# Kernel tuning notes

Measured on AMD Instinct MI355X. Metric: run time of the kernel, lower is better.

The kernel has to match this reference:

```python
import jax, jax.numpy as jnp
import numpy as np

N_NODES = 100000
N_EDGES = 200000
N_GRAPHS = 4096
NODE_DIM = 256
OUT_DIM = 768
LAYERS = 4
NODE_FEATS = 9
EDGE_FEATS = 3
NODE_VOCAB = 119  # max categorical size across node features (padded)
EDGE_VOCAB = 22   # max categorical size across edge features (padded)


def setup_inputs() -> dict:
    key = jax.random.key(0)
    ks = jax.random.split(key, 16)
    x_cat = jax.random.randint(ks[0], (N_NODES, NODE_FEATS), 0, 2)
    edge_attr = jax.random.randint(ks[1], (N_EDGES, EDGE_FEATS), 0, 2)
    edge_index = jax.random.randint(ks[2], (2, N_EDGES), 0, N_NODES)
    batch = jnp.sort(jax.random.randint(ks[3], (N_NODES,), 0, N_GRAPHS))
    s = 0.02
    node_emb = jax.random.normal(ks[4], (NODE_FEATS, NODE_VOCAB, NODE_DIM), jnp.float32) * s
    edge_emb = jax.random.normal(ks[5], (EDGE_FEATS, EDGE_VOCAB, NODE_DIM), jnp.float32) * s
    W1 = jax.random.normal(ks[6], (LAYERS, NODE_DIM, 2 * NODE_DIM), jnp.float32) * s
    b1 = jnp.zeros((LAYERS, 2 * NODE_DIM), jnp.float32)
    W2 = jax.random.normal(ks[7], (LAYERS, 2 * NODE_DIM, NODE_DIM), jnp.float32) * s
    b2 = jnp.zeros((LAYERS, NODE_DIM), jnp.float32)
    pW1 = jax.random.normal(ks[8], (NODE_DIM, NODE_DIM), jnp.float32) * s
    pb1 = jnp.zeros((NODE_DIM,), jnp.float32)
    pW2 = jax.random.normal(ks[9], (NODE_DIM, OUT_DIM), jnp.float32) * s
    pb2 = jnp.zeros((OUT_DIM,), jnp.float32)
    return {
        "x_cat": x_cat, "edge_attr": edge_attr, "edge_index": edge_index, "batch": batch,
        "node_emb": node_emb, "edge_emb": edge_emb,
        "W1": W1, "b1": b1, "W2": W2, "b2": b2,
        "pW1": pW1, "pb1": pb1, "pW2": pW2, "pb2": pb2,
    }


def _encode(tables, idx):
    # tables: [F, V, D], idx: [N, F] -> sum over features of embedding lookups -> [N, D]
    return jnp.sum(jax.vmap(lambda tbl, i: tbl[i], in_axes=(0, 1))(tables, idx), axis=0)


def reference(x_cat, edge_attr, edge_index, batch, node_emb, edge_emb,
              W1, b1, W2, b2, pW1, pb1, pW2, pb2):
    x = _encode(node_emb, x_cat)          # [N, D]
    e = _encode(edge_emb, edge_attr)      # [E, D]
    src, dst = edge_index[0], edge_index[1]
    for l in range(LAYERS):
        # GINEConv: aggr = sum_{j in N(i)} relu(x_j + e_ij); out = mlp((1+eps)*x_i + aggr), eps=0
        msg = jax.nn.relu(x[src] + e)                                  # [E, D]
        agg = jax.ops.segment_sum(msg, dst, num_segments=N_NODES)     # [N, D]
        h = x + agg
        h = jax.nn.relu(h @ W1[l] + b1[l]) @ W2[l] + b2[l]
        x = jax.nn.relu(h)
    g = jax.ops.segment_sum(x, batch, num_segments=N_GRAPHS)          # [G, D]
    g = jax.nn.relu(g @ pW1 + pb1) @ pW2 + pb2                         # [G, OUT]
    norm = jnp.maximum(jnp.linalg.norm(g, axis=-1, keepdims=True), 1e-12)
    return g / norm
```

## Files before the change

kernel.cpp:

```cpp
#include <hip/hip_runtime.h>

#define N_NODES 100000
#define N_NODES_PAD 100032
#define N_EDGES 200000
#define N_GRAPHS 4096
#define D 256
#define D2 512
#define OUTD 768
#define LAYERS 4
#define NODE_FEATS 9
#define EDGE_FEATS 3
#define NODE_VOCAB 119
#define EDGE_VOCAB 22
#define BM 64
#define GB 8

typedef __attribute__((ext_vector_type(8))) short bf16x8;
typedef __attribute__((ext_vector_type(4))) float f32x4;
typedef unsigned short ushort_t;
typedef unsigned int uint_t;

__device__ __forceinline__ ushort_t f2b(float f) {
    union { float f; uint_t u; } x; x.f = f;
    uint_t r = (x.u + 0x7FFFu + ((x.u >> 16) & 1u)) >> 16;
    return (ushort_t)r;
}
__device__ __forceinline__ float b2f(ushort_t u) {
    union { uint_t u; float f; } x; x.u = ((uint_t)u) << 16;
    return x.f;
}

__device__ __forceinline__ int lower_bound_i(const int* a, int n, int v) {
    int lo = 0, hi = n;
    while (lo < hi) { int mid = (lo + hi) >> 1; if (a[mid] < v) lo = mid + 1; else hi = mid; }
    return lo;
}

__global__ __launch_bounds__(256) void encode_nodes_k(const int* __restrict__ xcat,
                                                      const float* __restrict__ tab,
                                                      ushort_t* __restrict__ X) {
    int n = blockIdx.x, d = threadIdx.x;
    float acc = 0.f;
#pragma unroll
    for (int f = 0; f < NODE_FEATS; ++f) {
        int idx = xcat[n * NODE_FEATS + f];
        acc += tab[((size_t)f * NODE_VOCAB + idx) * D + d];
    }
    X[(size_t)n * D + d] = f2b(acc);
}

__global__ __launch_bounds__(256) void count_k(const int* __restrict__ eidx, int* deg) {
    int e = blockIdx.x * 256 + threadIdx.x;
    if (e < N_EDGES) atomicAdd(&deg[eidx[N_EDGES + e]], 1);
}

#define SCAN_B 1024
__global__ __launch_bounds__(256) void scan1_k(const int* __restrict__ deg,
                                               int* __restrict__ excl, int* __restrict__ bsum) {
    __shared__ int sh[256];
    int b = blockIdx.x, t = threadIdx.x;
    int base = b * SCAN_B + t * 4;
    int d0 = (base + 0) < N_NODES ? deg[base + 0] : 0;
    int d1 = (base + 1) < N_NODES ? deg[base + 1] : 0;
    int d2 = (base + 2) < N_NODES ? deg[base + 2] : 0;
    int d3 = (base + 3) < N_NODES ? deg[base + 3] : 0;
    int s = d0 + d1 + d2 + d3;
    sh[t] = s; __syncthreads();
    for (int off = 1; off < 256; off <<= 1) {
        int x = (t >= off) ? sh[t - off] : 0;
        __syncthreads();
        sh[t] += x;
        __syncthreads();
    }
    int incl = sh[t];
    int ex = incl - s;
    if (base + 0 < N_NODES) excl[base + 0] = ex;
    if (base + 1 < N_NODES) excl[base + 1] = ex + d0;
    if (base + 2 < N_NODES) excl[base + 2] = ex + d0 + d1;
    if (base + 3 < N_NODES) excl[base + 3] = ex + d0 + d1 + d2;
    if (t == 255) bsum[b] = incl;
}

__global__ void scan2_k(int* bsum, int nb) {
    __shared__ int sh[128];
    int t = threadIdx.x;
    int v = (t < nb) ? bsum[t] : 0;
    sh[t] = v; __syncthreads();
    for (int off = 1; off < 128; off <<= 1) {
        int x = (t >= off) ? sh[t - off] : 0;
        __syncthreads();
        sh[t] += x;
        __syncthreads();
    }
    if (t < nb) bsum[t] = sh[t] - v;
}

__global__ __launch_bounds__(256) void scan3_k(int* __restrict__ offs, int* __restrict__ cursor,
                                               const int* __restrict__ bsum) {
    int i = blockIdx.x * 256 + threadIdx.x;
    if (i < N_NODES) {
        int v = offs[i] + bsum[i >> 10];
        offs[i] = v;
        cursor[i] = v;
    }
}

__global__ __launch_bounds__(256) void fill_k(const int* __restrict__ eidx,
                                              const int* __restrict__ eattr,
                                              int* cursor, int2* __restrict__ elist) {
    int e = blockIdx.x * 256 + threadIdx.x;
    if (e < N_EDGES) {
        int src = eidx[e];
        int dst = eidx[N_EDGES + e];
        int pa = eattr[e * EDGE_FEATS + 0] | (eattr[e * EDGE_FEATS + 1] << 8)
               | (eattr[e * EDGE_FEATS + 2] << 16);
        int pos = atomicAdd(&cursor[dst], 1);
        elist[pos] = make_int2(src, pa);
    }
}

__global__ __launch_bounds__(256) void gather_k(const ushort4* __restrict__ X4,
                                                const float4* __restrict__ eemb4,
                                                const int* __restrict__ offs,
                                                const int* __restrict__ deg,
                                                const int2* __restrict__ elist,
                                                ushort4* __restrict__ H4) {
    int n = blockIdx.x * 4 + (threadIdx.x >> 6);
    int lane = threadIdx.x & 63;
    int start = offs[n], dg = deg[n];
    ushort4 xv = X4[(size_t)n * 64 + lane];
    float acc[4] = {b2f(xv.x), b2f(xv.y), b2f(xv.z), b2f(xv.w)};
    for (int i = 0; i < dg; ++i) {
        int2 sp = elist[start + i];
        ushort4 sv = X4[(size_t)sp.x * 64 + lane];
        float4 t0 = eemb4[(size_t)((sp.y      ) & 255) * 64 + lane];
        float4 t1 = eemb4[((size_t)EDGE_VOCAB + ((sp.y >> 8) & 255)) * 64 + lane];
        float4 t2 = eemb4[((size_t)2 * EDGE_VOCAB + ((sp.y >> 16) & 255)) * 64 + lane];
        acc[0] += fmaxf(b2f(sv.x) + t0.x + t1.x + t2.x, 0.f);
        acc[1] += fmaxf(b2f(sv.y) + t0.y + t1.y + t2.y, 0.f);
        acc[2] += fmaxf(b2f(sv.z) + t0.z + t1.z + t2.z, 0.f);
        acc[3] += fmaxf(b2f(sv.w) + t0.w + t1.w + t2.w, 0.f);
    }
    ushort4 hv;
    hv.x = f2b(acc[0]); hv.y = f2b(acc[1]); hv.z = f2b(acc[2]); hv.w = f2b(acc[3]);
    H4[(size_t)n * 64 + lane] = hv;
}

__global__ __launch_bounds__(256) void pack1_k(const float* __restrict__ W1, ushort_t* __restrict__ apack) {
    size_t i = (size_t)blockIdx.x * 256 + threadIdx.x;
    int l = (int)(i >> 14);
    int rem = (int)(i & 16383);
    int ntg = rem >> 9;
    int rem2 = rem & 511;
    int kk = rem2 >> 6;
    int lane = rem2 & 63;
    int n = ntg * 16 + (lane & 15);
    int k0 = kk * 32 + (lane >> 4) * 8;
    const float* w = W1 + ((size_t)l * D + k0) * D2 + n;
    ushort_t* o = apack + i * 8;
#pragma unroll
    for (int j = 0; j < 8; ++j) o[j] = f2b(w[(size_t)j * D2]);
}

__global__ __launch_bounds__(256) void pack2_k(const float* __restrict__ W2, ushort_t* __restrict__ bpack) {
    size_t i = (size_t)blockIdx.x * 256 + threadIdx.x;
    int l = (int)(i >> 14);
    int rem = (int)(i & 16383);
    int ntg = rem >> 10;
    int rem2 = rem & 1023;
    int kk = rem2 >> 6;
    int lane = rem2 & 63;
    int n = ntg * 16 + (lane & 15);
    int k0 = kk * 32 + (lane >> 4) * 8;
    const float* w = W2 + ((size_t)l * D2 + k0) * D + n;
    ushort_t* o = bpack + i * 8;
#pragma unroll
    for (int j = 0; j < 8; ++j) o[j] = f2b(w[(size_t)j * D]);
}

__global__ __launch_bounds__(512, 4) void mlp_k(const ushort_t* __restrict__ H,
                                                const ushort_t* __restrict__ apack,
                                                const float* __restrict__ b1,
                                                const ushort_t* __restrict__ bpack,
                                                const float* __restrict__ b2,
                                                ushort_t* __restrict__ X) {
    __shared__ __align__(16) char hA[BM * 512];
    __shared__ __align__(16) char midh[BM * 512];
    const int t = threadIdx.x;
    const int wid = t >> 6, lane = t & 63;
    const int l15 = lane & 15, g = lane >> 4;
    const size_t r0 = (size_t)blockIdx.x * BM;

    {
        const char* src = (const char*)(H + r0 * D);
#pragma unroll
        for (int c = 0; c < 4; ++c) {
            int Lb = (c * 512 + t) * 16;
            int row = Lb >> 9;
            int Sb = Lb ^ ((row & 7) << 4);
            *(uint4*)(hA + Sb) = *(const uint4*)(src + Lb);
        }
    }
    __syncthreads();

    f32x4 acc2[2][4];
#pragma unroll
    for (int a = 0; a < 2; ++a)
#pragma unroll
        for (int b = 0; b < 4; ++b) { f32x4 z = {0.f,0.f,0.f,0.f}; acc2[a][b] = z; }

#pragma unroll
    for (int half = 0; half < 2; ++half) {
        f32x4 acc1[2][4];
#pragma unroll
        for (int a = 0; a < 2; ++a)
#pragma unroll
            for (int b = 0; b < 4; ++b) { f32x4 z = {0.f,0.f,0.f,0.f}; acc1[a][b] = z; }

        bf16x8 AfA[2], AfB[2];
#pragma unroll
        for (int nt = 0; nt < 2; ++nt)
            AfA[nt] = *(const bf16x8*)(apack +
                ((size_t)((half * 16 + wid * 2 + nt) * 8 + 0) * 64 + lane) * 8);
#pragma unroll
        for (int kk = 0; kk < 8; ++kk) {
            bf16x8 Bf[4];
#pragma unroll
            for (int mt = 0; mt < 4; ++mt) {
                int m = mt * 16 + l15;
                Bf[mt] = *(const bf16x8*)(hA + ((m * 512 + (kk * 32 + g * 8) * 2) ^ ((m & 7) << 4)));
            }
            bf16x8* cur = (kk & 1) ? AfB : AfA;
            bf16x8* nxt = (kk & 1) ? AfA : AfB;
            if (kk < 7) {
#pragma unroll
                for (int nt = 0; nt < 2; ++nt)
                    nxt[nt] = *(const bf16x8*)(apack +
                        ((size_t)((half * 16 + wid * 2 + nt) * 8 + kk + 1) * 64 + lane) * 8);
            }
#pragma unroll
            for (int nt = 0; nt < 2; ++nt)
#pragma unroll
                for (int mt = 0; mt < 4; ++mt)
                    acc1[nt][mt] = __builtin_amdgcn_mfma_f32_16x16x32_bf16(cur[nt], Bf[mt], acc1[nt][mt], 0, 0, 0);
        }
#pragma unroll
        for (int nt = 0; nt < 2; ++nt) {
            int n0l = (wid * 2 + nt) * 16 + g * 4;
            f32x4 bv = *(const f32x4*)(b1 + half * 256 + n0l);
#pragma unroll
            for (int mt = 0; mt < 4; ++mt) {
                int m = mt * 16 + l15;
                ushort_t us[4];
#pragma unroll
                for (int r = 0; r < 4; ++r)
                    us[r] = f2b(fmaxf(acc1[nt][mt][r] + bv[r], 0.f));
                uint2 pk;
                pk.x = (uint_t)us[0] | ((uint_t)us[1] << 16);
                pk.y = (uint_t)us[2] | ((uint_t)us[3] << 16);
                *(uint2*)(midh + ((m * 512 + n0l * 2) ^ ((m & 7) << 4))) = pk;
            }
        }
        __syncthreads();

        bf16x8 WfA[2], WfB[2];
#pragma unroll
        for (int nt = 0; nt < 2; ++nt)
            WfA[nt] = *(const bf16x8*)(bpack +
                ((size_t)((wid * 2 + nt) * 16 + half * 8 + 0) * 64 + lane) * 8);
#pragma unroll
        for (int kk = 0; kk < 8; ++kk) {
            bf16x8 Mf[4];
#pragma unroll
            for (int mt = 0; mt < 4; ++mt) {
                int m = mt * 16 + l15;
                Mf[mt] = *(const bf16x8*)(midh + ((m * 512 + (kk * 32 + g * 8) * 2) ^ ((m & 7) << 4)));
            }
            bf16x8* cur = (kk & 1) ? WfB : WfA;
            bf16x8* nxt = (kk & 1) ? WfA : WfB;
            if (kk < 7) {
#pragma unroll
                for (int nt = 0; nt < 2; ++nt)
                    nxt[nt] = *(const bf16x8*)(bpack +
                        ((size_t)((wid * 2 + nt) * 16 + half * 8 + kk + 1) * 64 + lane) * 8);
            }
#pragma unroll
            for (int nt = 0; nt < 2; ++nt)
#pragma unroll
                for (int mt = 0; mt < 4; ++mt)
                    acc2[nt][mt] = __builtin_amdgcn_mfma_f32_16x16x32_bf16(cur[nt], Mf[mt], acc2[nt][mt], 0, 0, 0);
        }
        __syncthreads();
    }

#pragma unroll
    for (int nt = 0; nt < 2; ++nt) {
        int n0 = (wid * 2 + nt) * 16 + g * 4;
        f32x4 bv = *(const f32x4*)(b2 + n0);
#pragma unroll
        for (int mt = 0; mt < 4; ++mt) {
            int m = mt * 16 + l15;
            ushort_t us[4];
#pragma unroll
            for (int r = 0; r < 4; ++r)
                us[r] = f2b(fmaxf(acc2[nt][mt][r] + bv[r], 0.f));
            uint2 pk;
            pk.x = (uint_t)us[0] | ((uint_t)us[1] << 16);
            pk.y = (uint_t)us[2] | ((uint_t)us[3] << 16);
            *(uint2*)(X + (r0 + m) * D + n0) = pk;
        }
    }
}

__global__ __launch_bounds__(256) void final_k(const ushort_t* __restrict__ X,
                                               const int* __restrict__ batch,
                                               const float* __restrict__ pW1,
                                               const float* __restrict__ pb1,
                                               const float* __restrict__ pW2,
                                               const float* __restrict__ pb2,
                                               float* __restrict__ out) {
    __shared__ float gin[GB][D];
    __shared__ float mid[GB][D];
    __shared__ float red[GB][256];
    __shared__ int bnd[GB + 1];
    const int g0 = blockIdx.x * GB, t = threadIdx.x;
    if (t <= GB) bnd[t] = lower_bound_i(batch, N_NODES, g0 + t);
    __syncthreads();

#pragma unroll
    for (int q = 0; q < GB; ++q) {
        float a = 0.f;
        for (int n = bnd[q]; n < bnd[q + 1]; ++n)
            a += b2f(X[(size_t)n * D + t]);
        gin[q][t] = a;
    }
    __syncthreads();

    {
        float m_[GB];
        float bb = pb1[t];
#pragma unroll
        for (int q = 0; q < GB; ++q) m_[q] = bb;
        for (int k = 0; k < D; ++k) {
            float w = pW1[(size_t)k * D + t];
#pragma unroll
            for (int q = 0; q < GB; ++q) m_[q] += gin[q][k] * w;
        }
#pragma unroll
        for (int q = 0; q < GB; ++q) mid[q][t] = fmaxf(m_[q], 0.f);
    }
    __syncthreads();

    float a0[GB], a1[GB], a2[GB];
    {
        float b0 = pb2[t], b1_ = pb2[t + 256], b2_ = pb2[t + 512];
#pragma unroll
        for (int q = 0; q < GB; ++q) { a0[q] = b0; a1[q] = b1_; a2[q] = b2_; }
        for (int k = 0; k < D; ++k) {
            float w0 = pW2[(size_t)k * OUTD + t];
            float w1 = pW2[(size_t)k * OUTD + 256 + t];
            float w2 = pW2[(size_t)k * OUTD + 512 + t];
#pragma unroll
            for (int q = 0; q < GB; ++q) {
                float mv = mid[q][k];
                a0[q] += mv * w0; a1[q] += mv * w1; a2[q] += mv * w2;
            }
        }
    }
#pragma unroll
    for (int q = 0; q < GB; ++q)
        red[q][t] = a0[q] * a0[q] + a1[q] * a1[q] + a2[q] * a2[q];
    __syncthreads();
    for (int s = 128; s > 0; s >>= 1) {
        if (t < s) {
#pragma unroll
            for (int q = 0; q < GB; ++q) red[q][t] += red[q][t + s];
        }
        __syncthreads();
    }
#pragma unroll
    for (int q = 0; q < GB; ++q) {
        float inv = 1.f / fmaxf(sqrtf(red[q][0]), 1e-12f);
        out[(size_t)(g0 + q) * OUTD + t]       = a0[q] * inv;
        out[(size_t)(g0 + q) * OUTD + 256 + t] = a1[q] * inv;
        out[(size_t)(g0 + q) * OUTD + 512 + t] = a2[q] * inv;
    }
}

extern "C" void kernel_launch(void* const* d_in, const int* in_sizes, int n_in,
                              void* d_out, int out_size, void* d_ws, size_t ws_size,
                              hipStream_t stream) {
    const int*   x_cat      = (const int*)d_in[0];
    const int*   edge_attr  = (const int*)d_in[1];
    const int*   edge_index = (const int*)d_in[2];
    const int*   batch      = (const int*)d_in[3];
    const float* node_emb   = (const float*)d_in[4];
    const float* edge_emb   = (const float*)d_in[5];
    const float* W1  = (const float*)d_in[6];
    const float* b1  = (const float*)d_in[7];
    const float* W2  = (const float*)d_in[8];
    const float* b2  = (const float*)d_in[9];
    const float* pW1 = (const float*)d_in[10];
    const float* pb1 = (const float*)d_in[11];
    const float* pW2 = (const float*)d_in[12];
    const float* pb2 = (const float*)d_in[13];
    float* out = (float*)d_out;

    char* p = (char*)d_ws;
    auto carve = [&](size_t bytes) { char* q = p; p += (bytes + 255) & ~(size_t)255; return q; };
    ushort_t* X      = (ushort_t*)carve((size_t)N_NODES_PAD * D * 2);
    ushort_t* H      = (ushort_t*)carve((size_t)N_NODES_PAD * D * 2);
    int*      deg    = (int*)carve((size_t)N_NODES * 4);
    int*      offs   = (int*)carve((size_t)(N_NODES + 8) * 4);
    int*      cursor = (int*)carve((size_t)(N_NODES + 8) * 4);
    int*      bsum   = (int*)carve(1024);
    int2*     elist  = (int2*)carve((size_t)N_EDGES * 8);
    ushort_t* apack1 = (ushort_t*)carve((size_t)LAYERS * 32 * 8 * 64 * 8 * 2);
    ushort_t* bpack2 = (ushort_t*)carve((size_t)LAYERS * 16 * 16 * 64 * 8 * 2);

    const int NB = (N_NODES + SCAN_B - 1) / SCAN_B;

    pack1_k<<<256, 256, 0, stream>>>(W1, apack1);
    pack2_k<<<256, 256, 0, stream>>>(W2, bpack2);
    hipMemsetAsync(deg, 0, (size_t)N_NODES * 4, stream);
    count_k<<<(N_EDGES + 255) / 256, 256, 0, stream>>>(edge_index, deg);
    scan1_k<<<NB, 256, 0, stream>>>(deg, offs, bsum);
    scan2_k<<<1, 128, 0, stream>>>(bsum, NB);
    scan3_k<<<(N_NODES + 255) / 256, 256, 0, stream>>>(offs, cursor, bsum);
    fill_k<<<(N_EDGES + 255) / 256, 256, 0, stream>>>(edge_index, edge_attr, cursor, elist);

    encode_nodes_k<<<N_NODES, 256, 0, stream>>>(x_cat, node_emb, X);

    for (int l = 0; l < LAYERS; ++l) {
        gather_k<<<N_NODES / 4, 256, 0, stream>>>((const ushort4*)X, (const float4*)edge_emb,
                                                  offs, deg, elist, (ushort4*)H);
        mlp_k<<<(N_NODES_PAD) / BM, 512, 0, stream>>>(
            H,
            apack1 + (size_t)l * 32 * 8 * 64 * 8,
            b1 + (size_t)l * D2,
            bpack2 + (size_t)l * 16 * 16 * 64 * 8,
            b2 + (size_t)l * D,
            X);
    }

    final_k<<<N_GRAPHS / GB, 256, 0, stream>>>(X, batch, pW1, pb1, pW2, pb2, out);
}
```

Baseline: 751.2 us.

## Prefetch next edge in gather, hoist weight loads and raise MFMA priority, vectorize pooling

The gather kernel now software-pipelines the edge loop, loading the next edge's index and source row while the current edge's message is computed, so load latency is hidden. The MLP kernel issues its first weight-fragment loads before the barriers, letting them overlap the shared-memory staging and epilogue, and wraps the MFMA blocks in s_setprio so matrix work gets issue priority. The pooling step in final_k gives each wavefront one graph and reads four bf16 values per lane with a vector load instead of one scalar per thread per graph. These changes cost a few more live registers, which could lower occupancy.

```diff
diff --git a/kernel.cpp b/kernel.cpp
--- a/kernel.cpp
+++ b/kernel.cpp
@@ -130,16 +130,24 @@
     int start = offs[n], dg = deg[n];
     ushort4 xv = X4[(size_t)n * 64 + lane];
     float acc[4] = {b2f(xv.x), b2f(xv.y), b2f(xv.z), b2f(xv.w)};
-    for (int i = 0; i < dg; ++i) {
-        int2 sp = elist[start + i];
+    if (dg > 0) {
+        int2 sp = elist[start];
         ushort4 sv = X4[(size_t)sp.x * 64 + lane];
-        float4 t0 = eemb4[(size_t)((sp.y      ) & 255) * 64 + lane];
-        float4 t1 = eemb4[((size_t)EDGE_VOCAB + ((sp.y >> 8) & 255)) * 64 + lane];
-        float4 t2 = eemb4[((size_t)2 * EDGE_VOCAB + ((sp.y >> 16) & 255)) * 64 + lane];
-        acc[0] += fmaxf(b2f(sv.x) + t0.x + t1.x + t2.x, 0.f);
-        acc[1] += fmaxf(b2f(sv.y) + t0.y + t1.y + t2.y, 0.f);
-        acc[2] += fmaxf(b2f(sv.z) + t0.z + t1.z + t2.z, 0.f);
-        acc[3] += fmaxf(b2f(sv.w) + t0.w + t1.w + t2.w, 0.f);
+        for (int i = 0; i < dg; ++i) {
+            int2 spn = sp; ushort4 svn = sv;
+            if (i + 1 < dg) {
+                spn = elist[start + i + 1];
+                svn = X4[(size_t)spn.x * 64 + lane];
+            }
+            float4 t0 = eemb4[(size_t)((sp.y      ) & 255) * 64 + lane];
+            float4 t1 = eemb4[((size_t)EDGE_VOCAB + ((sp.y >> 8) & 255)) * 64 + lane];
+            float4 t2 = eemb4[((size_t)2 * EDGE_VOCAB + ((sp.y >> 16) & 255)) * 64 + lane];
+            acc[0] += fmaxf(b2f(sv.x) + t0.x + t1.x + t2.x, 0.f);
+            acc[1] += fmaxf(b2f(sv.y) + t0.y + t1.y + t2.y, 0.f);
+            acc[2] += fmaxf(b2f(sv.z) + t0.z + t1.z + t2.z, 0.f);
+            acc[3] += fmaxf(b2f(sv.w) + t0.w + t1.w + t2.w, 0.f);
+            sp = spn; sv = svn;
+        }
     }
     ushort4 hv;
     hv.x = f2b(acc[0]); hv.y = f2b(acc[1]); hv.z = f2b(acc[2]); hv.w = f2b(acc[3]);
@@ -201,13 +209,19 @@
             *(uint4*)(hA + Sb) = *(const uint4*)(src + Lb);
         }
     }
+
+    f32x4 acc2[2][4];
+#pragma unroll
+    for (int a = 0; a < 2; ++a)
+#pragma unroll
+        for (int b = 0; b < 4; ++b) { f32x4 z = {0.f,0.f,0.f,0.f}; acc2[a][b] = z; }
+
+    bf16x8 AfA[2], AfB[2], WfA[2], WfB[2];
+#pragma unroll
+    for (int nt = 0; nt < 2; ++nt)
+        AfA[nt] = *(const bf16x8*)(apack + ((size_t)((0 * 16 + wid * 2 + nt) * 8 + 0) * 64 + lane) * 8);
+
     __syncthreads();
-
-    f32x4 acc2[2][4];
-#pragma unroll
-    for (int a = 0; a < 2; ++a)
-#pragma unroll
-        for (int b = 0; b < 4; ++b) { f32x4 z = {0.f,0.f,0.f,0.f}; acc2[a][b] = z; }
 
 #pragma unroll
     for (int half = 0; half < 2; ++half) {
@@ -217,11 +231,6 @@
 #pragma unroll
             for (int b = 0; b < 4; ++b) { f32x4 z = {0.f,0.f,0.f,0.f}; acc1[a][b] = z; }
 
-        bf16x8 AfA[2], AfB[2];
-#pragma unroll
-        for (int nt = 0; nt < 2; ++nt)
-            AfA[nt] = *(const bf16x8*)(apack +
-                ((size_t)((half * 16 + wid * 2 + nt) * 8 + 0) * 64 + lane) * 8);
 #pragma unroll
         for (int kk = 0; kk < 8; ++kk) {
             bf16x8 Bf[4];
@@ -238,12 +247,20 @@
                     nxt[nt] = *(const bf16x8*)(apack +
                         ((size_t)((half * 16 + wid * 2 + nt) * 8 + kk + 1) * 64 + lane) * 8);
             }
+            __builtin_amdgcn_s_setprio(1);
 #pragma unroll
             for (int nt = 0; nt < 2; ++nt)
 #pragma unroll
                 for (int mt = 0; mt < 4; ++mt)
                     acc1[nt][mt] = __builtin_amdgcn_mfma_f32_16x16x32_bf16(cur[nt], Bf[mt], acc1[nt][mt], 0, 0, 0);
-        }
+            __builtin_amdgcn_s_setprio(0);
+        }
+
+#pragma unroll
+        for (int nt = 0; nt < 2; ++nt)
+            WfA[nt] = *(const bf16x8*)(bpack +
+                ((size_t)((wid * 2 + nt) * 16 + half * 8 + 0) * 64 + lane) * 8);
+
 #pragma unroll
         for (int nt = 0; nt < 2; ++nt) {
             int n0l = (wid * 2 + nt) * 16 + g * 4;
@@ -263,11 +280,6 @@
         }
         __syncthreads();
 
-        bf16x8 WfA[2], WfB[2];
-#pragma unroll
-        for (int nt = 0; nt < 2; ++nt)
-            WfA[nt] = *(const bf16x8*)(bpack +
-                ((size_t)((wid * 2 + nt) * 16 + half * 8 + 0) * 64 + lane) * 8);
 #pragma unroll
         for (int kk = 0; kk < 8; ++kk) {
             bf16x8 Mf[4];
@@ -284,11 +296,20 @@
                     nxt[nt] = *(const bf16x8*)(bpack +
                         ((size_t)((wid * 2 + nt) * 16 + half * 8 + kk + 1) * 64 + lane) * 8);
             }
+            __builtin_amdgcn_s_setprio(1);
 #pragma unroll
             for (int nt = 0; nt < 2; ++nt)
 #pragma unroll
                 for (int mt = 0; mt < 4; ++mt)
                     acc2[nt][mt] = __builtin_amdgcn_mfma_f32_16x16x32_bf16(cur[nt], Mf[mt], acc2[nt][mt], 0, 0, 0);
+            __builtin_amdgcn_s_setprio(0);
+        }
+
+        if (half == 0) {
+#pragma unroll
+            for (int nt = 0; nt < 2; ++nt)
+                AfA[nt] = *(const bf16x8*)(apack +
+                    ((size_t)((1 * 16 + wid * 2 + nt) * 8 + 0) * 64 + lane) * 8);
         }
         __syncthreads();
     }
@@ -312,7 +333,7 @@
     }
 }
 
-__global__ __launch_bounds__(256) void final_k(const ushort_t* __restrict__ X,
+__global__ __launch_bounds__(256) void final_k(const ushort4* __restrict__ X4,
                                                const int* __restrict__ batch,
                                                const float* __restrict__ pW1,
                                                const float* __restrict__ pb1,
@@ -324,15 +345,19 @@
     __shared__ float red[GB][256];
     __shared__ int bnd[GB + 1];
     const int g0 = blockIdx.x * GB, t = threadIdx.x;
+    const int wid = t >> 6, lane = t & 63;
     if (t <= GB) bnd[t] = lower_bound_i(batch, N_NODES, g0 + t);
     __syncthreads();
 
 #pragma unroll
-    for (int q = 0; q < GB; ++q) {
-        float a = 0.f;
-        for (int n = bnd[q]; n < bnd[q + 1]; ++n)
-            a += b2f(X[(size_t)n * D + t]);
-        gin[q][t] = a;
+    for (int qq = 0; qq < 2; ++qq) {
+        int q = wid + qq * 4;
+        f32x4 a = {0.f, 0.f, 0.f, 0.f};
+        for (int n = bnd[q]; n < bnd[q + 1]; ++n) {
+            ushort4 v = X4[(size_t)n * 64 + lane];
+            a.x += b2f(v.x); a.y += b2f(v.y); a.z += b2f(v.z); a.w += b2f(v.w);
+        }
+        *(f32x4*)&gin[q][lane * 4] = a;
     }
     __syncthreads();
 
@@ -443,5 +468,5 @@
             X);
     }
 
-    final_k<<<N_GRAPHS / GB, 256, 0, stream>>>(X, batch, pW1, pb1, pW2, pb2, out);
-}
+    final_k<<<N_GRAPHS / GB, 256, 0, stream>>>((const ushort4*)X, batch, pW1, pb1, pW2, pb2, out);
+}
```

Result: faster. 713.5 us (-5.0%).
